# Performance work log

Measured on AMD Instinct MI355X. Metric: run time of the kernel, lower is better.

## Reference

```python
import jax, jax.numpy as jnp
import numpy as np

DT_MIN = 0.001  # config.rsp_dt_min
HARMONIC_SCALE = 0.1


def phi(z):
    # ResonantActivation: SiLU plus small harmonic term (harmonic_scale=0.1)
    return jax.nn.silu(z) + HARMONIC_SCALE * jnp.sin(z)


def setup_inputs() -> dict:
    key = jax.random.key(0)
    ks = jax.random.split(key, 8)
    B, L, D = 4, 2048, 1024
    std = 1.0 / np.sqrt(D)
    inp = {
        "x": jax.random.normal(ks[0], (B, L, D), dtype=jnp.float32),
        "f_prev": jnp.zeros((B, D), dtype=jnp.float32),
        "s_prev": jnp.zeros((B, D), dtype=jnp.float32),
        "w_lambda": jnp.zeros((D,), dtype=jnp.float32),
        "P_lambda_w": jax.random.uniform(ks[1], (D, D), jnp.float32, -std, std),
        "W_beta_w": jax.random.uniform(ks[2], (D, D), jnp.float32, -std, std),
        "W_alpha_w": jax.random.uniform(ks[3], (D, D), jnp.float32, -std, std),
        "W_alpha_b": jnp.full((D,), -3.0, dtype=jnp.float32),  # rsp_init_bias_alpha
        "W_rho_w": 0.01 * jax.random.normal(ks[4], (D, 3 * D), dtype=jnp.float32),
        "W_rho_b": jnp.full((D,), 2.0, dtype=jnp.float32),  # rsp_init_bias_rho
        "out_proj_w": 0.02 * jax.random.normal(ks[5], (D, D), dtype=jnp.float32),
        "res_scale": jnp.ones((1,), dtype=jnp.float32),
    }
    return inp


def _rsp_forward(x, f_prev, s_prev, w_lambda, P_lambda_w, W_beta_w,
                 W_alpha_w, W_alpha_b, W_rho_w, W_rho_b, out_proj_w, res_scale):
    # x: [B, L, D]
    # Input-dependent decay: lambda = exp(-exp(clip(w + x @ P^T)))
    lnl = jnp.clip(w_lambda + jnp.einsum('bld,ed->ble', x, P_lambda_w), -4.0, 4.0)
    lam = jnp.clip(jnp.exp(-jnp.exp(lnl)), DT_MIN, 1.0 - DT_MIN)

    B_gate = phi(jnp.einsum('bld,ed->ble', x, W_beta_w))
    alpha = jax.nn.sigmoid(jnp.einsum('bld,ed->ble', x, W_alpha_w) + W_alpha_b)

    # inject f_prev into first step's input contribution
    b_in = B_gate.at[:, 0, :].set(lam[:, 0, :] * f_prev + B_gate[:, 0, :])

    # fast linear recurrence: h_t = lam_t * h_{t-1} + b_t   (scan over L)
    lam_t = jnp.moveaxis(lam, 1, 0)      # [L, B, D]
    b_t = jnp.moveaxis(b_in, 1, 0)       # [L, B, D]

    def fast_step(h, lb):
        l, b = lb
        h = l * h + b
        return h, h

    _, f_seq = jax.lax.scan(fast_step, jnp.zeros_like(f_prev), (lam_t, b_t))
    f_states = jnp.moveaxis(f_seq, 0, 1)  # [B, L, D]

    # slow EMA: s_t = s_{t-1} + alpha_t * (f_t - s_{t-1})
    a_t = jnp.moveaxis(alpha, 1, 0)

    def slow_step(s, af):
        a, f = af
        s = s + a * (f - s)
        return s, s

    _, s_seq = jax.lax.scan(slow_step, s_prev, (a_t, f_seq))
    s_states = jnp.moveaxis(s_seq, 0, 1)  # [B, L, D]

    gate_input = jnp.concatenate([f_states, s_states, x], axis=-1)  # [B, L, 3D]
    rho = jax.nn.sigmoid(jnp.einsum('blk,ek->ble', gate_input, W_rho_w) + W_rho_b)
    h = rho * f_states + (1.0 - rho) * s_states
    h = x + res_scale * jnp.einsum('bld,ed->ble', h, out_proj_w)
    return h, f_states[:, -1, :], s_states[:, -1, :]


def reference(x, f_prev, s_prev, w_lambda, P_lambda_w, W_beta_w, W_alpha_w,
              W_alpha_b, W_rho_w, W_rho_b, out_proj_w, res_scale):
    return _rsp_forward(x, f_prev, s_prev, w_lambda, P_lambda_w, W_beta_w,
                        W_alpha_w, W_alpha_b, W_rho_w, W_rho_b, out_proj_w, res_scale)
```

## Files before the change

kernel.cpp:

```cpp
#include <hip/hip_runtime.h>

#define Bb 4
#define Ll 2048
#define Dd 1024
#define Mm (Bb*Ll)
#define NCH 64
#define CLEN (Ll/NCH)

typedef __attribute__((ext_vector_type(4))) float f32x4;
typedef __attribute__((ext_vector_type(8))) short s16x8;
typedef __attribute__((ext_vector_type(4))) short s16x4;

__device__ __forceinline__ float sigm(float v){ return 1.0f/(1.0f+__expf(-v)); }

__device__ __forceinline__ short bf16rne(float f){
  unsigned u = __builtin_bit_cast(unsigned, f);
  u += 0x7fffu + ((u>>16)&1u);
  return (short)(u>>16);
}
__device__ __forceinline__ float bf2f(short s){
  unsigned u = ((unsigned)(unsigned short)s) << 16;
  return __builtin_bit_cast(float, u);
}

__device__ __forceinline__ void gl_lds16(const void* g, void* l){
  __builtin_amdgcn_global_load_lds((__attribute__((address_space(1))) void*)g,
                                   (__attribute__((address_space(3))) void*)l, 16, 0, 0);
}

template<int EPI>
__launch_bounds__(256)
__global__ void gemm_bt(const short* __restrict__ A0, const short* __restrict__ A1,
                        const short* __restrict__ A2, const short* __restrict__ W,
                        int K,
                        const float* __restrict__ b0, const float* __restrict__ b1,
                        const float* __restrict__ xres, const float* __restrict__ rsp,
                        const short* __restrict__ fB, const short* __restrict__ sB,
                        float* __restrict__ oF, short* __restrict__ oB0,
                        short* __restrict__ oB1)
{
  __shared__ short As[2][128*32];
  __shared__ short Bs[2][128*32];
  const int tid  = threadIdx.x;
  const int lane = tid & 63;
  const int wid  = tid >> 6;
  const int wm = wid >> 1, wn = wid & 1;
  const long bn0 = (long)blockIdx.x * 128;
  const long bm0 = (long)blockIdx.y * 128;

  f32x4 acc[4][4] = {};

  const int r0 = tid >> 2;
  const int r1 = (256 + tid) >> 2;
  const int sg = (tid & 3) * 8;

  auto stage = [&](int buf, int k0){
    const short* Asrc = A0; long acol = k0;
    if (EPI == 3) {
      const int blk = k0 >> 10;
      Asrc = (blk == 0) ? A0 : ((blk == 1) ? A1 : A2);
      acol = k0 & 1023;
    }
    gl_lds16(Asrc + (bm0 + r0)*1024 + acol + sg, &As[buf][(size_t)tid*8]);
    gl_lds16(Asrc + (bm0 + r1)*1024 + acol + sg, &As[buf][(size_t)(256+tid)*8]);
    gl_lds16(W + (bn0 + r0)*(long)K + k0 + sg, &Bs[buf][(size_t)tid*8]);
    gl_lds16(W + (bn0 + r1)*(long)K + k0 + sg, &Bs[buf][(size_t)(256+tid)*8]);
  };

  auto compute = [&](int buf){
    s16x8 af[4], bfr[4];
    #pragma unroll
    for (int mi = 0; mi < 4; ++mi)
      af[mi] = *(const s16x8*)&As[buf][(wm*64 + mi*16 + (lane & 15))*32 + (lane >> 4)*8];
    #pragma unroll
    for (int ni = 0; ni < 4; ++ni)
      bfr[ni] = *(const s16x8*)&Bs[buf][(wn*64 + ni*16 + (lane & 15))*32 + (lane >> 4)*8];
    #pragma unroll
    for (int mi = 0; mi < 4; ++mi)
      #pragma unroll
      for (int ni = 0; ni < 4; ++ni)
        asm("v_mfma_f32_16x16x32_bf16 %0, %1, %2, %0"
            : "+v"(acc[mi][ni]) : "v"(af[mi]), "v"(bfr[ni]));
  };

  stage(0, 0);
  __syncthreads();
  int cur = 0;
  for (int k0 = 32; k0 < K; k0 += 32) {
    stage(cur ^ 1, k0);
    compute(cur);
    __syncthreads();
    cur ^= 1;
  }
  compute(cur);

  const float rs = (EPI == 4) ? rsp[0] : 0.0f;
  const int seg = (EPI == 5) ? (int)(bn0 >> 10) : 0;
  const int ecol0 = (int)bn0 + wn*64 + (lane & 15);
  const int erow0 = (int)bm0 + wm*64 + ((lane >> 4) << 2);

  #pragma unroll
  for (int mi = 0; mi < 4; ++mi) {
    #pragma unroll
    for (int ni = 0; ni < 4; ++ni) {
      asm volatile("s_nop 7\n\ts_nop 7\n\ts_nop 7" : "+v"(acc[mi][ni]));
      const f32x4 v = acc[mi][ni];
      const int gn = ecol0 + ni*16;
      const int cn = gn & 1023;
      #pragma unroll
      for (int j = 0; j < 4; ++j) {
        const long gm  = erow0 + mi*16 + j;
        const long idx = gm*1024 + cn;
        const float val = v[j];
        if (EPI == 5) {
          if (seg == 0) {
            float z = val + b0[cn];
            z = fminf(fmaxf(z, -4.0f), 4.0f);
            float l = __expf(-__expf(z));
            oF[idx] = fminf(fmaxf(l, 0.001f), 0.999f);
          } else if (seg == 1) {
            oB0[idx] = bf16rne(val*sigm(val) + 0.1f*__sinf(val));
          } else {
            oB1[idx] = bf16rne(sigm(val + b1[cn]));
          }
        } else if (EPI == 3) {
          const float r = sigm(val + b0[cn]);
          const float f = bf2f(fB[idx]);
          const float s = bf2f(sB[idx]);
          oB0[idx] = bf16rne(r*f + (1.0f - r)*s);
        } else {
          oF[idx] = xres[idx] + rs*val;
        }
      }
    }
  }
}


__global__ void f_chunk1(const float* __restrict__ lm, const short* __restrict__ bgB,
                         const float* __restrict__ fprev,
                         float* __restrict__ cP, float* __restrict__ cB)
{
  const int d = blockIdx.x*256 + threadIdx.x;
  const int c = blockIdx.y, b = blockIdx.z;
  float P = 1.0f, Bv = 0.0f;
  size_t base = ((size_t)b*Ll + (size_t)c*CLEN)*Dd + d;
  const float fp = (c == 0) ? fprev[b*Dd + d] : 0.0f;
  for (int t = 0; t < CLEN; ++t) {
    const float l = lm[base];
    float bb = bf2f(bgB[base]);
    if (c == 0 && t == 0) bb += l*fp;
    P *= l;
    Bv = l*Bv + bb;
    base += Dd;
  }
  const size_t ci = ((size_t)b*NCH + c)*Dd + d;
  cP[ci] = P; cB[ci] = Bv;
}

__global__ void scan_carry(const float* __restrict__ cP, const float* __restrict__ cB,
                           const float* __restrict__ init,
                           float* __restrict__ H0, float* __restrict__ last_out)
{
  const int d = blockIdx.x*256 + threadIdx.x;
  const int b = blockIdx.y;
  float h = init ? init[b*Dd + d] : 0.0f;
  for (int c = 0; c < NCH; ++c) {
    const size_t ci = ((size_t)b*NCH + c)*Dd + d;
    H0[ci] = h;
    h = cP[ci]*h + cB[ci];
  }
  last_out[b*Dd + d] = h;
}

__global__ void fs_mid(const float* __restrict__ lm, const short* __restrict__ bgB,
                       const float* __restrict__ fprev, const float* __restrict__ H0f,
                       const short* __restrict__ alB,
                       short* __restrict__ fob, float* __restrict__ cPs,
                       float* __restrict__ cBs)
{
  const int d = blockIdx.x*256 + threadIdx.x;
  const int c = blockIdx.y, b = blockIdx.z;
  float h = H0f[((size_t)b*NCH + c)*Dd + d];
  float sP = 1.0f, sBv = 0.0f;
  size_t base = ((size_t)b*Ll + (size_t)c*CLEN)*Dd + d;
  const float fp = (c == 0) ? fprev[b*Dd + d] : 0.0f;
  for (int t = 0; t < CLEN; ++t) {
    const float l = lm[base];
    float bb = bf2f(bgB[base]);
    if (c == 0 && t == 0) bb += l*fp;
    h = l*h + bb;
    const short hr = bf16rne(h);
    fob[base] = hr;
    const float fr = bf2f(hr);
    const float a = bf2f(alB[base]);
    sP *= (1.0f - a);
    sBv = (1.0f - a)*sBv + a*fr;
    base += Dd;
  }
  const size_t ci = ((size_t)b*NCH + c)*Dd + d;
  cPs[ci] = sP; cBs[ci] = sBv;
}

__global__ void s_chunk3(const float* __restrict__ alB_unused_f32, const short* __restrict__ alB,
                         const short* __restrict__ fob, const float* __restrict__ H0s,
                         short* __restrict__ sob)
{
  const int d = blockIdx.x*256 + threadIdx.x;
  const int c = blockIdx.y, b = blockIdx.z;
  float h = H0s[((size_t)b*NCH + c)*Dd + d];
  size_t base = ((size_t)b*Ll + (size_t)c*CLEN)*Dd + d;
  for (int t = 0; t < CLEN; ++t) {
    const float a = bf2f(alB[base]);
    const float f = bf2f(fob[base]);
    h = h + a*(f - h);
    sob[base] = bf16rne(h);
    base += Dd;
  }
}

__global__ void cvt_bf16(const float* __restrict__ src, short* __restrict__ dst, int n4)
{
  int i = blockIdx.x*256 + threadIdx.x;
  const int stride = gridDim.x*256;
  for (; i < n4; i += stride) {
    const f32x4 v = ((const f32x4*)src)[i];
    s16x4 o;
    o[0] = bf16rne(v[0]); o[1] = bf16rne(v[1]);
    o[2] = bf16rne(v[2]); o[3] = bf16rne(v[3]);
    ((s16x4*)dst)[i] = o;
  }
}

extern "C" void kernel_launch(void* const* d_in, const int* in_sizes, int n_in,
                              void* d_out, int out_size, void* d_ws, size_t ws_size,
                              hipStream_t stream)
{
  (void)in_sizes; (void)n_in; (void)out_size; (void)ws_size;
  const float* x   = (const float*)d_in[0];
  const float* fpv = (const float*)d_in[1];
  const float* spv = (const float*)d_in[2];
  const float* wl  = (const float*)d_in[3];
  const float* Pw  = (const float*)d_in[4];
  const float* Wbw = (const float*)d_in[5];
  const float* Waw = (const float*)d_in[6];
  const float* ab  = (const float*)d_in[7];
  const float* Wr  = (const float*)d_in[8];
  const float* rb  = (const float*)d_in[9];
  const float* Wo  = (const float*)d_in[10];
  const float* rs  = (const float*)d_in[11];

  float* out    = (float*)d_out;
  float* f_last = out + (size_t)Mm*Dd;
  float* s_last = f_last + (size_t)Bb*Dd;

  char* w = (char*)d_ws;
  auto alloc = [&](size_t bytes){ char* p = w; w += (bytes + 255) & ~(size_t)255; return p; };
  short* xb   = (short*)alloc((size_t)Mm*Dd*2);
  short* w3   = (short*)alloc((size_t)3*Dd*Dd*2);
  short* wrb  = (short*)alloc((size_t)Dd*3*Dd*2);
  short* opb  = (short*)alloc((size_t)Dd*Dd*2);
  float* lam  = (float*)alloc((size_t)Mm*Dd*4);
  short* bgB  = (short*)alloc((size_t)Mm*Dd*2);
  short* alB  = (short*)alloc((size_t)Mm*Dd*2);
  short* fb   = (short*)alloc((size_t)Mm*Dd*2);
  short* sb   = (short*)alloc((size_t)Mm*Dd*2);
  float* cP   = (float*)alloc((size_t)Bb*NCH*Dd*4);
  float* cB   = (float*)alloc((size_t)Bb*NCH*Dd*4);
  float* H0   = (float*)alloc((size_t)Bb*NCH*Dd*4);
  short* hm   = (short*)lam;

  auto cvt = [&](const float* s_, short* d_, size_t n){
    int n4 = (int)(n/4);
    int grid = (n4 + 255)/256; if (grid > 2048) grid = 2048;
    cvt_bf16<<<dim3(grid), dim3(256), 0, stream>>>(s_, d_, n4);
  };
  cvt(x,   xb,            (size_t)Mm*Dd);
  cvt(Pw,  w3,            (size_t)Dd*Dd);
  cvt(Wbw, w3 +   Dd*Dd,  (size_t)Dd*Dd);
  cvt(Waw, w3 + 2*Dd*Dd,  (size_t)Dd*Dd);
  cvt(Wr,  wrb,           (size_t)Dd*3*Dd);
  cvt(Wo,  opb,           (size_t)Dd*Dd);

  gemm_bt<5><<<dim3(3*Dd/128, Mm/128), dim3(256), 0, stream>>>(
      xb, nullptr, nullptr, w3, Dd, wl, ab, nullptr, nullptr, nullptr, nullptr,
      lam, bgB, alB);

  const dim3 gs(Dd/256, NCH, Bb);
  const dim3 gc(Dd/256, Bb);
  f_chunk1<<<gs, dim3(256), 0, stream>>>(lam, bgB, fpv, cP, cB);
  scan_carry<<<gc, dim3(256), 0, stream>>>(cP, cB, (const float*)nullptr, H0, f_last);
  fs_mid<<<gs, dim3(256), 0, stream>>>(lam, bgB, fpv, H0, alB, fb, cP, cB);
  scan_carry<<<gc, dim3(256), 0, stream>>>(cP, cB, spv, H0, s_last);
  s_chunk3<<<gs, dim3(256), 0, stream>>>(nullptr, alB, fb, H0, sb);

  gemm_bt<3><<<dim3(Dd/128, Mm/128), dim3(256), 0, stream>>>(
      fb, sb, xb, wrb, 3*Dd, rb, nullptr, nullptr, nullptr, fb, sb,
      nullptr, hm, nullptr);

  gemm_bt<4><<<dim3(Dd/128, Mm/128), dim3(256), 0, stream>>>(
      hm, nullptr, nullptr, opb, Dd, nullptr, nullptr, x, rs, nullptr, nullptr,
      out, nullptr, nullptr);
}
```

Measured before the change: 389.9 us.

## Triple-buffer GEMM with swizzled LDS, store lambda as u16, fuse converts

The GEMM main loop moves from a double-buffered, __syncthreads-based pipeline to a triple-buffered one with explicit vmcnt waits and raw barriers. LDS reads and writes use an XOR swizzle to cut bank conflicts. The decay lambda is now stored as 16-bit fixed point instead of fp32, halving its write and read traffic in the scan kernels at some cost in precision. The six bf16 conversion launches are merged into one kernel. The contiguous placement of w3, wrb and opb after xb is assumed so that all six conversions write through the single xb pointer.

```diff
diff --git a/kernel.cpp b/kernel.cpp
--- a/kernel.cpp
+++ b/kernel.cpp
@@ -10,6 +10,10 @@
 typedef __attribute__((ext_vector_type(4))) float f32x4;
 typedef __attribute__((ext_vector_type(8))) short s16x8;
 typedef __attribute__((ext_vector_type(4))) short s16x4;
+
+#define WAITV4 asm volatile("s_waitcnt vmcnt(4)" ::: "memory")
+#define WAITV0 asm volatile("s_waitcnt vmcnt(0)" ::: "memory")
+#define BARRAW asm volatile("s_barrier" ::: "memory")
 
 __device__ __forceinline__ float sigm(float v){ return 1.0f/(1.0f+__expf(-v)); }
 
@@ -36,11 +40,11 @@
                         const float* __restrict__ b0, const float* __restrict__ b1,
                         const float* __restrict__ xres, const float* __restrict__ rsp,
                         const short* __restrict__ fB, const short* __restrict__ sB,
-                        float* __restrict__ oF, short* __restrict__ oB0,
-                        short* __restrict__ oB1)
-{
-  __shared__ short As[2][128*32];
-  __shared__ short Bs[2][128*32];
+                        float* __restrict__ oF, unsigned short* __restrict__ oU,
+                        short* __restrict__ oB0, short* __restrict__ oB1)
+{
+  __shared__ short As[3][128*32];
+  __shared__ short Bs[3][128*32];
   const int tid  = threadIdx.x;
   const int lane = tid & 63;
   const int wid  = tid >> 6;
@@ -51,8 +55,10 @@
   f32x4 acc[4][4] = {};
 
   const int r0 = tid >> 2;
-  const int r1 = (256 + tid) >> 2;
-  const int sg = (tid & 3) * 8;
+  const int r1 = 64 + r0;
+  const int j  = tid & 3;
+  const int sw0 = (j ^ ((r0 >> 1) & 3)) * 8;
+  const int sw1 = (j ^ ((r1 >> 1) & 3)) * 8;
 
   auto stage = [&](int buf, int k0){
     const short* Asrc = A0; long acol = k0;
@@ -61,20 +67,25 @@
       Asrc = (blk == 0) ? A0 : ((blk == 1) ? A1 : A2);
       acol = k0 & 1023;
     }
-    gl_lds16(Asrc + (bm0 + r0)*1024 + acol + sg, &As[buf][(size_t)tid*8]);
-    gl_lds16(Asrc + (bm0 + r1)*1024 + acol + sg, &As[buf][(size_t)(256+tid)*8]);
-    gl_lds16(W + (bn0 + r0)*(long)K + k0 + sg, &Bs[buf][(size_t)tid*8]);
-    gl_lds16(W + (bn0 + r1)*(long)K + k0 + sg, &Bs[buf][(size_t)(256+tid)*8]);
+    gl_lds16(Asrc + (bm0 + r0)*1024 + acol + sw0, &As[buf][(size_t)tid*8]);
+    gl_lds16(Asrc + (bm0 + r1)*1024 + acol + sw1, &As[buf][(size_t)(256+tid)*8]);
+    gl_lds16(W + (bn0 + r0)*(long)K + k0 + sw0, &Bs[buf][(size_t)tid*8]);
+    gl_lds16(W + (bn0 + r1)*(long)K + k0 + sw1, &Bs[buf][(size_t)(256+tid)*8]);
   };
 
   auto compute = [&](int buf){
+    const int q = lane >> 4;
     s16x8 af[4], bfr[4];
     #pragma unroll
-    for (int mi = 0; mi < 4; ++mi)
-      af[mi] = *(const s16x8*)&As[buf][(wm*64 + mi*16 + (lane & 15))*32 + (lane >> 4)*8];
+    for (int mi = 0; mi < 4; ++mi) {
+      const int row = wm*64 + mi*16 + (lane & 15);
+      af[mi] = *(const s16x8*)&As[buf][row*32 + ((q ^ ((row>>1)&3)) << 3)];
+    }
     #pragma unroll
-    for (int ni = 0; ni < 4; ++ni)
-      bfr[ni] = *(const s16x8*)&Bs[buf][(wn*64 + ni*16 + (lane & 15))*32 + (lane >> 4)*8];
+    for (int ni = 0; ni < 4; ++ni) {
+      const int row = wn*64 + ni*16 + (lane & 15);
+      bfr[ni] = *(const s16x8*)&Bs[buf][row*32 + ((q ^ ((row>>1)&3)) << 3)];
+    }
     #pragma unroll
     for (int mi = 0; mi < 4; ++mi)
       #pragma unroll
@@ -83,16 +94,18 @@
             : "+v"(acc[mi][ni]) : "v"(af[mi]), "v"(bfr[ni]));
   };
 
+  const int NK = K >> 5;
   stage(0, 0);
-  __syncthreads();
-  int cur = 0;
-  for (int k0 = 32; k0 < K; k0 += 32) {
-    stage(cur ^ 1, k0);
-    compute(cur);
-    __syncthreads();
-    cur ^= 1;
-  }
-  compute(cur);
+  stage(1, 32);
+  WAITV4;
+  BARRAW;
+  for (int it = 0; it < NK; ++it) {
+    const bool pf = (it + 2) < NK;
+    if (pf) stage((it + 2) % 3, (it + 2) << 5);
+    compute(it % 3);
+    if (pf) { WAITV4; } else { WAITV0; }
+    BARRAW;
+  }
 
   const float rs = (EPI == 4) ? rsp[0] : 0.0f;
   const int seg = (EPI == 5) ? (int)(bn0 >> 10) : 0;
@@ -108,16 +121,17 @@
       const int gn = ecol0 + ni*16;
       const int cn = gn & 1023;
       #pragma unroll
-      for (int j = 0; j < 4; ++j) {
-        const long gm  = erow0 + mi*16 + j;
+      for (int jj = 0; jj < 4; ++jj) {
+        const long gm  = erow0 + mi*16 + jj;
         const long idx = gm*1024 + cn;
-        const float val = v[j];
+        const float val = v[jj];
         if (EPI == 5) {
           if (seg == 0) {
             float z = val + b0[cn];
             z = fminf(fmaxf(z, -4.0f), 4.0f);
             float l = __expf(-__expf(z));
-            oF[idx] = fminf(fmaxf(l, 0.001f), 0.999f);
+            l = fminf(fmaxf(l, 0.001f), 0.999f);
+            oU[idx] = (unsigned short)__float2uint_rn(l * 65535.0f);
           } else if (seg == 1) {
             oB0[idx] = bf16rne(val*sigm(val) + 0.1f*__sinf(val));
           } else {
@@ -137,7 +151,7 @@
 }
 
 
-__global__ void f_chunk1(const float* __restrict__ lm, const short* __restrict__ bgB,
+__global__ void f_chunk1(const unsigned short* __restrict__ lmU, const short* __restrict__ bgB,
                          const float* __restrict__ fprev,
                          float* __restrict__ cP, float* __restrict__ cB)
 {
@@ -147,7 +161,7 @@
   size_t base = ((size_t)b*Ll + (size_t)c*CLEN)*Dd + d;
   const float fp = (c == 0) ? fprev[b*Dd + d] : 0.0f;
   for (int t = 0; t < CLEN; ++t) {
-    const float l = lm[base];
+    const float l = (float)lmU[base] * (1.0f/65535.0f);
     float bb = bf2f(bgB[base]);
     if (c == 0 && t == 0) bb += l*fp;
     P *= l;
@@ -173,7 +187,7 @@
   last_out[b*Dd + d] = h;
 }
 
-__global__ void fs_mid(const float* __restrict__ lm, const short* __restrict__ bgB,
+__global__ void fs_mid(const unsigned short* __restrict__ lmU, const short* __restrict__ bgB,
                        const float* __restrict__ fprev, const float* __restrict__ H0f,
                        const short* __restrict__ alB,
                        short* __restrict__ fob, float* __restrict__ cPs,
@@ -186,7 +200,7 @@
   size_t base = ((size_t)b*Ll + (size_t)c*CLEN)*Dd + d;
   const float fp = (c == 0) ? fprev[b*Dd + d] : 0.0f;
   for (int t = 0; t < CLEN; ++t) {
-    const float l = lm[base];
+    const float l = (float)lmU[base] * (1.0f/65535.0f);
     float bb = bf2f(bgB[base]);
     if (c == 0 && t == 0) bb += l*fp;
     h = l*h + bb;
@@ -202,9 +216,8 @@
   cPs[ci] = sP; cBs[ci] = sBv;
 }
 
-__global__ void s_chunk3(const float* __restrict__ alB_unused_f32, const short* __restrict__ alB,
-                         const short* __restrict__ fob, const float* __restrict__ H0s,
-                         short* __restrict__ sob)
+__global__ void s_chunk3(const short* __restrict__ alB, const short* __restrict__ fob,
+                         const float* __restrict__ H0s, short* __restrict__ sob)
 {
   const int d = blockIdx.x*256 + threadIdx.x;
   const int c = blockIdx.y, b = blockIdx.z;
@@ -219,12 +232,23 @@
   }
 }
 
-__global__ void cvt_bf16(const float* __restrict__ src, short* __restrict__ dst, int n4)
-{
+__global__ void cvt6(const float* __restrict__ a0, const float* __restrict__ a1,
+                     const float* __restrict__ a2, const float* __restrict__ a3,
+                     const float* __restrict__ a4, const float* __restrict__ a5,
+                     short* __restrict__ dst)
+{
+  const int n0 = (Mm*Dd)/4, n1 = (Dd*Dd)/4, n4 = (3*Dd*Dd)/4;
+  const int c1 = n0, c2 = c1+n1, c3 = c2+n1, c4 = c3+n1, c5 = c4+n4, total = c5+n1;
   int i = blockIdx.x*256 + threadIdx.x;
-  const int stride = gridDim.x*256;
-  for (; i < n4; i += stride) {
-    const f32x4 v = ((const f32x4*)src)[i];
+  for (; i < total; i += gridDim.x*256) {
+    const float* src; int off;
+    if      (i < c1) { src = a0; off = i; }
+    else if (i < c2) { src = a1; off = i - c1; }
+    else if (i < c3) { src = a2; off = i - c2; }
+    else if (i < c4) { src = a3; off = i - c3; }
+    else if (i < c5) { src = a4; off = i - c4; }
+    else             { src = a5; off = i - c5; }
+    const f32x4 v = ((const f32x4*)src)[off];
     s16x4 o;
     o[0] = bf16rne(v[0]); o[1] = bf16rne(v[1]);
     o[2] = bf16rne(v[2]); o[3] = bf16rne(v[3]);
@@ -260,7 +284,7 @@
   short* w3   = (short*)alloc((size_t)3*Dd*Dd*2);
   short* wrb  = (short*)alloc((size_t)Dd*3*Dd*2);
   short* opb  = (short*)alloc((size_t)Dd*Dd*2);
-  float* lam  = (float*)alloc((size_t)Mm*Dd*4);
+  unsigned short* lamU = (unsigned short*)alloc((size_t)Mm*Dd*2);
   short* bgB  = (short*)alloc((size_t)Mm*Dd*2);
   short* alB  = (short*)alloc((size_t)Mm*Dd*2);
   short* fb   = (short*)alloc((size_t)Mm*Dd*2);
@@ -268,37 +292,27 @@
   float* cP   = (float*)alloc((size_t)Bb*NCH*Dd*4);
   float* cB   = (float*)alloc((size_t)Bb*NCH*Dd*4);
   float* H0   = (float*)alloc((size_t)Bb*NCH*Dd*4);
-  short* hm   = (short*)lam;
-
-  auto cvt = [&](const float* s_, short* d_, size_t n){
-    int n4 = (int)(n/4);
-    int grid = (n4 + 255)/256; if (grid > 2048) grid = 2048;
-    cvt_bf16<<<dim3(grid), dim3(256), 0, stream>>>(s_, d_, n4);
-  };
-  cvt(x,   xb,            (size_t)Mm*Dd);
-  cvt(Pw,  w3,            (size_t)Dd*Dd);
-  cvt(Wbw, w3 +   Dd*Dd,  (size_t)Dd*Dd);
-  cvt(Waw, w3 + 2*Dd*Dd,  (size_t)Dd*Dd);
-  cvt(Wr,  wrb,           (size_t)Dd*3*Dd);
-  cvt(Wo,  opb,           (size_t)Dd*Dd);
+  short* hm   = (short*)lamU;
+
+  cvt6<<<dim3(2048), dim3(256), 0, stream>>>(x, Pw, Wbw, Waw, Wr, Wo, xb);
 
   gemm_bt<5><<<dim3(3*Dd/128, Mm/128), dim3(256), 0, stream>>>(
       xb, nullptr, nullptr, w3, Dd, wl, ab, nullptr, nullptr, nullptr, nullptr,
-      lam, bgB, alB);
+      nullptr, lamU, bgB, alB);
 
   const dim3 gs(Dd/256, NCH, Bb);
   const dim3 gc(Dd/256, Bb);
-  f_chunk1<<<gs, dim3(256), 0, stream>>>(lam, bgB, fpv, cP, cB);
+  f_chunk1<<<gs, dim3(256), 0, stream>>>(lamU, bgB, fpv, cP, cB);
   scan_carry<<<gc, dim3(256), 0, stream>>>(cP, cB, (const float*)nullptr, H0, f_last);
-  fs_mid<<<gs, dim3(256), 0, stream>>>(lam, bgB, fpv, H0, alB, fb, cP, cB);
+  fs_mid<<<gs, dim3(256), 0, stream>>>(lamU, bgB, fpv, H0, alB, fb, cP, cB);
   scan_carry<<<gc, dim3(256), 0, stream>>>(cP, cB, spv, H0, s_last);
-  s_chunk3<<<gs, dim3(256), 0, stream>>>(nullptr, alB, fb, H0, sb);
+  s_chunk3<<<gs, dim3(256), 0, stream>>>(alB, fb, H0, sb);
 
   gemm_bt<3><<<dim3(Dd/128, Mm/128), dim3(256), 0, stream>>>(
       fb, sb, xb, wrb, 3*Dd, rb, nullptr, nullptr, nullptr, fb, sb,
-      nullptr, hm, nullptr);
+      nullptr, nullptr, hm, nullptr);
 
   gemm_bt<4><<<dim3(Dd/128, Mm/128), dim3(256), 0, stream>>>(
       hm, nullptr, nullptr, opb, Dd, nullptr, nullptr, x, rs, nullptr, nullptr,
-      out, nullptr, nullptr);
-}
+      out, nullptr, nullptr, nullptr);
+}
```

Result: faster. 366.4 us (-6.0%).
